# Performance work log

Measured on AMD Instinct MI355X. Metric: run time of the kernel, lower is better.

## Reference

```python
import jax, jax.numpy as jnp
import numpy as np

DN = ('NCDHW', 'OIDHW', 'NCDHW')  # torch Conv3d layout

def conv3d(x, w, b, pad):
    y = jax.lax.conv_general_dilated(x, w, (1, 1, 1), [(p, p) for p in pad], dimension_numbers=DN)
    return y + b[None, :, None, None, None]

def setup_inputs() -> dict:
    key = jax.random.key(0)
    ks = jax.random.split(key, 10)
    C, Cq = 64, 8  # in_channels, in_channels // 8
    s = 0.05
    x = jax.random.normal(ks[0], (2, C, 16, 16, 16), dtype=jnp.float32)
    return {
        'x': x,
        'wq': jax.random.normal(ks[1], (Cq, C, 1, 3, 1), jnp.float32) * s,
        'bq': jax.random.normal(ks[2], (Cq,), jnp.float32) * s,
        'wk': jax.random.normal(ks[3], (Cq, C, 3, 1, 1), jnp.float32) * s,
        'bk': jax.random.normal(ks[4], (Cq,), jnp.float32) * s,
        'wj': jax.random.normal(ks[5], (Cq, C, 1, 1, 3), jnp.float32) * s,
        'bj': jax.random.normal(ks[6], (Cq,), jnp.float32) * s,
        'wv': jax.random.normal(ks[7], (C, C, 1, 1, 1), jnp.float32) * s,
        'bv': jax.random.normal(ks[8], (C,), jnp.float32) * s,
        'gamma': jax.random.normal(ks[9], (1,), jnp.float32) * s,
    }

def reference(x, wq, bq, wk, bk, wj, bj, wv, bv, gamma):
    B, C, H, W, D = x.shape
    N = H * W * D
    q = conv3d(x, wq, bq, (0, 1, 0)).reshape(B, -1, N)   # [B, c, N]
    k = conv3d(x, wk, bk, (1, 0, 0)).reshape(B, -1, N)   # [B, c, N]
    j = conv3d(x, wj, bj, (0, 0, 1)).reshape(B, -1, N)   # [B, c, N]
    # affinity = (Q^T K) (J^T K) reassociated as Q^T (K J^T) K  -- identical math,
    # O(N^2 c) instead of O(N^3) since c = C//8 << N.
    kj = jnp.einsum('bcn,bdn->bcd', k, j)                # [B, c, c] = K @ J^T
    aff = jnp.einsum('bcn,bcd,bdm->bnm', q, kj, k)       # [B, N, N]
    aff = jax.nn.softmax(aff, axis=-1)
    v = conv3d(x, wv, bv, (0, 0, 0)).reshape(B, C, N)    # [B, C, N]
    weights = jnp.einsum('bcn,bnm->bcm', v, aff).reshape(B, C, H, W, D)
    return gamma * weights + x
```

## Files before the change

### kernel.cpp

```cpp
#include <hip/hip_runtime.h>

#define N 4096
#define CIN 64
#define NB 2

typedef unsigned short u16;
typedef short bf16x8 __attribute__((ext_vector_type(8)));
typedef float f32x4 __attribute__((ext_vector_type(4)));

#define OFF_QT 0
#define OFF_KT (OFF_QT + NB*N*8)
#define OFF_JT (OFF_KT + NB*N*8)
#define OFF_V  (OFF_JT + NB*N*8)
#define OFF_QK (OFF_V + NB*CIN*N)
#define OFF_MX (OFF_QK + NB*N*8)
#define OFF_SC (OFF_MX + NB*N)
#define OFF_KJ (OFF_SC + NB*N)

__device__ __forceinline__ u16 f2bf(float f) {
    union { float f; unsigned u; } v; v.f = f;
    unsigned r = (v.u + 0x7fffu + ((v.u >> 16) & 1u)) >> 16;
    return (u16)r;
}

__global__ __launch_bounds__(512, 4) void prep(
        const float* __restrict__ x,
        const float* __restrict__ wq, const float* __restrict__ bq,
        const float* __restrict__ wk, const float* __restrict__ bk,
        const float* __restrict__ wj, const float* __restrict__ bj,
        const float* __restrict__ wv, const float* __restrict__ bv,
        float* __restrict__ ws, u16* __restrict__ vbf, float* __restrict__ out) {
    __shared__ union {
        float kj2[2][8][256];
        float q1[8][256];
        float accv[256][8];
    } sh;
    __shared__ float kjpart[4][64];
    const int t    = threadIdx.x;
    const int tn   = t & 255;
    const int half = t >> 8;
    const int y    = blockIdx.y;
    const int bx   = blockIdx.x;
    const int b    = blockIdx.z;
    const int n    = bx * 256 + tn;
    const float* xb = x + (size_t)b * CIN * N + n;
    const int c0base = half * 32;

    if (y == 8) {
        const int lane = t & 63, wid = t >> 6;
        int d = n & 15, h = n >> 8;
        int ohl = (h > 0) ? -256 : 0, ohh = (h < 15) ? 256 : 0;
        int odl = (d > 0) ? -1 : 0,   odh = (d < 15) ? 1 : 0;
        float mhl = (h > 0) ? 1.f : 0.f, mhh = (h < 15) ? 1.f : 0.f;
        float mdl = (d > 0) ? 1.f : 0.f, mdh = (d < 15) ? 1.f : 0.f;
        float k[8], j[8];
#pragma unroll
        for (int cq = 0; cq < 8; ++cq) {
            k[cq] = half ? 0.f : bk[cq];
            j[cq] = half ? 0.f : bj[cq];
        }
        for (int c0i = 0; c0i < 32; c0i += 4) {
            const int c0 = c0base + c0i;
            float xc[4], xhl[4], xhh[4], xdl[4], xdh[4];
#pragma unroll
            for (int u = 0; u < 4; ++u) {
                const float* p = xb + (size_t)(c0 + u) * N;
                xc[u]  = p[0];
                xhl[u] = p[ohl]; xhh[u] = p[ohh];
                xdl[u] = p[odl]; xdh[u] = p[odh];
            }
#pragma unroll
            for (int u = 0; u < 4; ++u) {
                xhl[u] *= mhl; xhh[u] *= mhh;
                xdl[u] *= mdl; xdh[u] *= mdh;
            }
#pragma unroll
            for (int cq = 0; cq < 8; ++cq) {
                const float4* wk4 = (const float4*)(wk + (cq * CIN + c0) * 3);
                float4 ka4 = wk4[0], kb4 = wk4[1], kc4 = wk4[2];
                k[cq] += ka4.x * xhl[0] + ka4.y * xc[0] + ka4.z * xhh[0]
                       + ka4.w * xhl[1] + kb4.x * xc[1] + kb4.y * xhh[1]
                       + kb4.z * xhl[2] + kb4.w * xc[2] + kc4.x * xhh[2]
                       + kc4.y * xhl[3] + kc4.z * xc[3] + kc4.w * xhh[3];
                const float4* wj4 = (const float4*)(wj + (cq * CIN + c0) * 3);
                float4 ja4 = wj4[0], jb4 = wj4[1], jc4 = wj4[2];
                j[cq] += ja4.x * xdl[0] + ja4.y * xc[0] + ja4.z * xdh[0]
                       + ja4.w * xdl[1] + jb4.x * xc[1] + jb4.y * xdh[1]
                       + jb4.z * xdl[2] + jb4.w * xc[2] + jc4.x * xdh[2]
                       + jc4.y * xdl[3] + jc4.z * xc[3] + jc4.w * xdh[3];
            }
        }
        if (half) {
#pragma unroll
            for (int cq = 0; cq < 8; ++cq) {
                sh.kj2[0][cq][tn] = k[cq];
                sh.kj2[1][cq][tn] = j[cq];
            }
        }
        __syncthreads();
        if (!half) {
#pragma unroll
            for (int cq = 0; cq < 8; ++cq) {
                k[cq] += sh.kj2[0][cq][tn];
                j[cq] += sh.kj2[1][cq][tn];
            }
            size_t base = (size_t)(b * N + n) * 8;
#pragma unroll
            for (int cq = 0; cq < 8; ++cq) {
                ws[OFF_KT + base + cq] = k[cq];
                ws[OFF_JT + base + cq] = j[cq];
            }
#pragma unroll
            for (int g = 0; g < 4; ++g) {
                float a16[16];
#pragma unroll
                for (int cc = 0; cc < 2; ++cc)
#pragma unroll
                    for (int dd = 0; dd < 8; ++dd)
                        a16[cc * 8 + dd] = k[g * 2 + cc] * j[dd];
#pragma unroll
                for (int s = 32; s >= 1; s >>= 1)
#pragma unroll
                    for (int i = 0; i < 16; ++i) a16[i] += __shfl_down(a16[i], s, 64);
                if (lane == 0) {
#pragma unroll
                    for (int i = 0; i < 16; ++i) kjpart[wid][g * 16 + i] = a16[i];
                }
            }
        }
        __syncthreads();
        if (t < 64) {
            float s = kjpart[0][t] + kjpart[1][t] + kjpart[2][t] + kjpart[3][t];
            ws[OFF_KJ + (size_t)(b * 16 + bx) * 64 + t] = s;
        }
    } else if (y == 9) {
        int w = (n >> 4) & 15;
        int owl = (w > 0) ? -16 : 0, owh = (w < 15) ? 16 : 0;
        float mwl = (w > 0) ? 1.f : 0.f, mwh = (w < 15) ? 1.f : 0.f;
        float q[8];
#pragma unroll
        for (int cq = 0; cq < 8; ++cq) q[cq] = half ? 0.f : bq[cq];
        for (int c0i = 0; c0i < 32; c0i += 8) {
            const int c0 = c0base + c0i;
            float xc[8], xwl[8], xwh[8];
#pragma unroll
            for (int u = 0; u < 8; ++u) {
                const float* p = xb + (size_t)(c0 + u) * N;
                xc[u] = p[0]; xwl[u] = p[owl]; xwh[u] = p[owh];
            }
#pragma unroll
            for (int u = 0; u < 8; ++u) { xwl[u] *= mwl; xwh[u] *= mwh; }
#pragma unroll
            for (int cq = 0; cq < 8; ++cq) {
                const float4* w4 = (const float4*)(wq + (cq * CIN + c0) * 3);
                float4 a4 = w4[0], b4 = w4[1], c4 = w4[2],
                       d4 = w4[3], e4 = w4[4], f4 = w4[5];
                q[cq] += a4.x * xwl[0] + a4.y * xc[0] + a4.z * xwh[0]
                       + a4.w * xwl[1] + b4.x * xc[1] + b4.y * xwh[1]
                       + b4.z * xwl[2] + b4.w * xc[2] + c4.x * xwh[2]
                       + c4.y * xwl[3] + c4.z * xc[3] + c4.w * xwh[3]
                       + d4.x * xwl[4] + d4.y * xc[4] + d4.z * xwh[4]
                       + d4.w * xwl[5] + e4.x * xc[5] + e4.y * xwh[5]
                       + e4.z * xwl[6] + e4.w * xc[6] + f4.x * xwh[6]
                       + f4.y * xwl[7] + f4.z * xc[7] + f4.w * xwh[7];
            }
        }
        if (half) {
#pragma unroll
            for (int cq = 0; cq < 8; ++cq) sh.q1[cq][tn] = q[cq];
        }
        __syncthreads();
        if (!half) {
            size_t base = (size_t)(b * N + n) * 8;
#pragma unroll
            for (int cq = 0; cq < 8; ++cq)
                ws[OFF_QT + base + cq] = q[cq] + sh.q1[cq][tn];
        }
    } else {
        int yy = y;
        int co0 = yy * 8;
        float acc[8];
#pragma unroll
        for (int i = 0; i < 8; ++i) acc[i] = half ? 0.f : bv[co0 + i];
        for (int c0i = 0; c0i < 32; c0i += 8) {
            const int c0 = c0base + c0i;
            float xv[8];
#pragma unroll
            for (int u = 0; u < 8; ++u) xv[u] = xb[(size_t)(c0 + u) * N];
#pragma unroll
            for (int u = 0; u < 8; ++u)
#pragma unroll
                for (int i = 0; i < 8; ++i)
                    acc[i] += wv[(co0 + i) * CIN + c0 + u] * xv[u];
            if ((c0 >> 3) == yy) {
#pragma unroll
                for (int u = 0; u < 8; ++u)
                    out[(size_t)(b * CIN + c0 + u) * N + n] = xv[u];
            }
        }
        if (half) {
#pragma unroll
            for (int i = 0; i < 8; ++i) sh.accv[tn][i] = acc[i];
        }
        __syncthreads();
        if (!half) {
#pragma unroll
            for (int i = 0; i < 8; ++i)
                vbf[(size_t)(b * CIN + co0 + i) * N + n] = f2bf(acc[i] + sh.accv[tn][i]);
        }
    }
}

__global__ __launch_bounds__(512, 4) void pass1(const float* __restrict__ ws_in,
                                                float* __restrict__ ws,
                                                const float* __restrict__ gamma) {
    __shared__ float kjs[64];
    __shared__ float smx[8][4];
    __shared__ float ssum[8][4];
    const int t = threadIdx.x, lane = t & 63, wid = t >> 6;
    const int r0 = blockIdx.x * 4;
    const int b  = r0 >> 12;
    const float* ktb = ws_in + OFF_KT + (size_t)b * N * 8;

    if (t < 64) {
        const float* kjw = ws_in + OFF_KJ + (size_t)b * 16 * 64;
        float s = 0.f;
#pragma unroll
        for (int p = 0; p < 16; ++p) s += kjw[p * 64 + t];
        kjs[t] = s;
    }
    __syncthreads();

    float4 qa[4], qb[4];
#pragma unroll
    for (int rr = 0; rr < 4; ++rr) {
        const float4* q4 = (const float4*)(ws_in + OFF_QT + (size_t)(r0 + rr) * 8);
        float4 a4 = q4[0], b4 = q4[1];
        float qv[8] = {a4.x, a4.y, a4.z, a4.w, b4.x, b4.y, b4.z, b4.w};
        float o[8];
#pragma unroll
        for (int dd = 0; dd < 8; ++dd) {
            float a = 0.f;
#pragma unroll
            for (int c = 0; c < 8; ++c) a += qv[c] * kjs[c * 8 + dd];
            o[dd] = a;
        }
        qa[rr] = make_float4(o[0], o[1], o[2], o[3]);
        qb[rr] = make_float4(o[4], o[5], o[6], o[7]);
    }
    if (wid == 0 && lane < 32) {
        const int rr = lane >> 3, dd = lane & 7;
        const float* qr = ws_in + OFF_QT + (size_t)(r0 + rr) * 8;
        float o = 0.f;
#pragma unroll
        for (int c = 0; c < 8; ++c) o += qr[c] * kjs[c * 8 + dd];
        ws[OFF_QK + (size_t)r0 * 8 + lane] = o;
    }

    float as[4][8];
#pragma unroll
    for (int i = 0; i < 8; ++i) {
        const int m = wid * 512 + i * 64 + lane;
        const float4* kk4 = (const float4*)(ktb + (size_t)m * 8);
        float4 ka = kk4[0], kb2 = kk4[1];
#pragma unroll
        for (int rr = 0; rr < 4; ++rr)
            as[rr][i] = qa[rr].x * ka.x + qa[rr].y * ka.y + qa[rr].z * ka.z + qa[rr].w * ka.w
                      + qb[rr].x * kb2.x + qb[rr].y * kb2.y + qb[rr].z * kb2.z + qb[rr].w * kb2.w;
    }

    float mx[4];
#pragma unroll
    for (int rr = 0; rr < 4; ++rr) {
        float m01 = fmaxf(fmaxf(as[rr][0], as[rr][1]), fmaxf(as[rr][2], as[rr][3]));
        float m23 = fmaxf(fmaxf(as[rr][4], as[rr][5]), fmaxf(as[rr][6], as[rr][7]));
        mx[rr] = fmaxf(m01, m23);
    }
#pragma unroll
    for (int s = 32; s >= 1; s >>= 1)
#pragma unroll
        for (int rr = 0; rr < 4; ++rr)
            mx[rr] = fmaxf(mx[rr], __shfl_xor(mx[rr], s, 64));
    if (lane == 0) {
#pragma unroll
        for (int rr = 0; rr < 4; ++rr) smx[wid][rr] = mx[rr];
    }
    __syncthreads();
    float gm[4];
#pragma unroll
    for (int rr = 0; rr < 4; ++rr) {
        float g0 = fmaxf(fmaxf(smx[0][rr], smx[1][rr]), fmaxf(smx[2][rr], smx[3][rr]));
        float g1 = fmaxf(fmaxf(smx[4][rr], smx[5][rr]), fmaxf(smx[6][rr], smx[7][rr]));
        gm[rr] = fmaxf(g0, g1);
    }

    float sm[4];
#pragma unroll
    for (int rr = 0; rr < 4; ++rr) {
        float s0 = __expf(as[rr][0] - gm[rr]) + __expf(as[rr][1] - gm[rr])
                 + __expf(as[rr][2] - gm[rr]) + __expf(as[rr][3] - gm[rr]);
        float s1 = __expf(as[rr][4] - gm[rr]) + __expf(as[rr][5] - gm[rr])
                 + __expf(as[rr][6] - gm[rr]) + __expf(as[rr][7] - gm[rr]);
        sm[rr] = s0 + s1;
    }
#pragma unroll
    for (int s = 32; s >= 1; s >>= 1)
#pragma unroll
        for (int rr = 0; rr < 4; ++rr)
            sm[rr] += __shfl_xor(sm[rr], s, 64);
    if (lane == 0) {
#pragma unroll
        for (int rr = 0; rr < 4; ++rr) ssum[wid][rr] = sm[rr];
    }
    __syncthreads();
    if (t < 4) {
        float g0 = fmaxf(fmaxf(smx[0][t], smx[1][t]), fmaxf(smx[2][t], smx[3][t]));
        float g1 = fmaxf(fmaxf(smx[4][t], smx[5][t]), fmaxf(smx[6][t], smx[7][t]));
        float g  = fmaxf(g0, g1);
        float tt = ((ssum[0][t] + ssum[1][t]) + (ssum[2][t] + ssum[3][t]))
                 + ((ssum[4][t] + ssum[5][t]) + (ssum[6][t] + ssum[7][t]));
        ws[OFF_MX + r0 + t] = g;
        ws[OFF_SC + r0 + t] = gamma[0] / tt;
    }
}

__global__ __launch_bounds__(256) void pass2(const float* __restrict__ ws,
                                             const u16* __restrict__ vbf,
                                             float* __restrict__ out) {
    __shared__ u16 Pt[64][72];
    __shared__ u16 Vt[64][72];
    __shared__ float ks[64][8];
    const int t  = threadIdx.x;
    const int b  = blockIdx.z;
    const int m0 = blockIdx.x * 64;
    const int ns = blockIdx.y;
    const float* qkT = ws + OFF_QK + (size_t)b * N * 8;
    const float* ktb = ws + OFF_KT + (size_t)b * N * 8;
    const float* mxv = ws + OFF_MX + (size_t)b * N;
    const float* scv = ws + OFF_SC + (size_t)b * N;
    const u16*   vb  = vbf + (size_t)b * CIN * N;

    if (t < 128) ((float4*)ks)[t] = ((const float4*)(ktb + (size_t)m0 * 8))[t];

    const int lane = t & 63;
    const int wid  = t >> 6;
    const int l16  = lane & 15;
    const int lq   = lane >> 4;
    const int vc   = t >> 3;
    const int vseg = t & 7;

    f32x4 acc[4];
#pragma unroll
    for (int i = 0; i < 4; ++i) acc[i] = (f32x4){0.f, 0.f, 0.f, 0.f};

    for (int ch = 0; ch < 8; ++ch) {
        const int n0 = ns * 512 + ch * 64;
        const int n  = n0 + lane;
        const float4* q4 = (const float4*)(qkT + (size_t)n * 8);
        float4 qa = q4[0], qb = q4[1];
        float mxl = mxv[n], sl = scv[n];
        uint4 v0 = *(const uint4*)(vb + (size_t)vc        * N + n0 + vseg * 8);
        uint4 v1 = *(const uint4*)(vb + (size_t)(vc + 32) * N + n0 + vseg * 8);
        __syncthreads();
#pragma unroll
        for (int r = 0; r < 16; ++r) {
            int mi = wid * 16 + r;
            float4 k0 = *(const float4*)&ks[mi][0];
            float4 k1 = *(const float4*)&ks[mi][4];
            float a = qa.x * k0.x + qa.y * k0.y + qa.z * k0.z + qa.w * k0.w
                    + qb.x * k1.x + qb.y * k1.y + qb.z * k1.z + qb.w * k1.w;
            Pt[mi][lane] = f2bf(__expf(a - mxl) * sl);
        }
        *(uint4*)&Vt[vc][vseg * 8]      = v0;
        *(uint4*)&Vt[vc + 32][vseg * 8] = v1;
        __syncthreads();
#pragma unroll
        for (int kk = 0; kk < 2; ++kk) {
            int k0i = kk * 32 + lq * 8;
            bf16x8 bfrag = *(const bf16x8*)&Pt[wid * 16 + l16][k0i];
#pragma unroll
            for (int ct = 0; ct < 4; ++ct) {
                bf16x8 afrag = *(const bf16x8*)&Vt[ct * 16 + l16][k0i];
                acc[ct] = __builtin_amdgcn_mfma_f32_16x16x32_bf16(afrag, bfrag, acc[ct], 0, 0, 0);
            }
        }
    }
    float* ob = out + (size_t)b * CIN * N;
    const int mcol = m0 + wid * 16 + l16;
#pragma unroll
    for (int ct = 0; ct < 4; ++ct)
#pragma unroll
        for (int r = 0; r < 4; ++r) {
            int c = ct * 16 + lq * 4 + r;
            atomicAdd(&ob[(size_t)c * N + mcol], acc[ct][r]);
        }
}

extern "C" void kernel_launch(void* const* d_in, const int* in_sizes, int n_in,
                              void* d_out, int out_size, void* d_ws, size_t ws_size,
                              hipStream_t stream) {
    const float* x  = (const float*)d_in[0];
    const float* wq = (const float*)d_in[1];
    const float* bq = (const float*)d_in[2];
    const float* wk = (const float*)d_in[3];
    const float* bk = (const float*)d_in[4];
    const float* wj = (const float*)d_in[5];
    const float* bj = (const float*)d_in[6];
    const float* wv = (const float*)d_in[7];
    const float* bv = (const float*)d_in[8];
    const float* gamma = (const float*)d_in[9];
    float* ws  = (float*)d_ws;
    float* out = (float*)d_out;
    u16* vbf = (u16*)(ws + OFF_V);

    prep<<<dim3(16, 10, 2), 512, 0, stream>>>(x, wq, bq, wk, bk, wj, bj, wv, bv, ws, vbf, out);
    pass1<<<2048, 512, 0, stream>>>(ws, ws, gamma);
    pass2<<<dim3(64, 8, 2), 256, 0, stream>>>(ws, vbf, out);
}
```

Before: 160.2 us.

## Split Q/K/J conv blocks into 64-point tiles with 8-way channel split

```diff
diff --git a/kernel.cpp b/kernel.cpp
--- a/kernel.cpp
+++ b/kernel.cpp
@@ -31,78 +31,120 @@
         const float* __restrict__ wv, const float* __restrict__ bv,
         float* __restrict__ ws, u16* __restrict__ vbf, float* __restrict__ out) {
     __shared__ union {
-        float kj2[2][8][256];
-        float q1[8][256];
+        float ab[2][8][8][64];
         float accv[256][8];
     } sh;
-    __shared__ float kjpart[4][64];
-    const int t    = threadIdx.x;
-    const int tn   = t & 255;
-    const int half = t >> 8;
-    const int y    = blockIdx.y;
-    const int bx   = blockIdx.x;
-    const int b    = blockIdx.z;
-    const int n    = bx * 256 + tn;
-    const float* xb = x + (size_t)b * CIN * N + n;
-    const int c0base = half * 32;
-
-    if (y == 8) {
-        const int lane = t & 63, wid = t >> 6;
+    const int t   = threadIdx.x;
+    const int blk = blockIdx.x;
+    const int b   = blk >> 8;
+    const int r   = blk & 255;
+
+    if (r < 128) {
+        const int tn   = t & 255;
+        const int half = t >> 8;
+        const int yy   = r >> 4;
+        const int bx   = r & 15;
+        const int n    = bx * 256 + tn;
+        const float* xb = x + (size_t)b * CIN * N + n;
+        const int c0base = half * 32;
+        int co0 = yy * 8;
+        float acc[8];
+#pragma unroll
+        for (int i = 0; i < 8; ++i) acc[i] = half ? 0.f : bv[co0 + i];
+        for (int c0i = 0; c0i < 32; c0i += 8) {
+            const int c0 = c0base + c0i;
+            float xv[8];
+#pragma unroll
+            for (int u = 0; u < 8; ++u) xv[u] = xb[(size_t)(c0 + u) * N];
+#pragma unroll
+            for (int u = 0; u < 8; ++u)
+#pragma unroll
+                for (int i = 0; i < 8; ++i)
+                    acc[i] += wv[(co0 + i) * CIN + c0 + u] * xv[u];
+            if ((c0 >> 3) == yy) {
+#pragma unroll
+                for (int u = 0; u < 8; ++u)
+                    out[(size_t)(b * CIN + c0 + u) * N + n] = xv[u];
+            }
+        }
+        if (half) {
+#pragma unroll
+            for (int i = 0; i < 8; ++i) sh.accv[tn][i] = acc[i];
+        }
+        __syncthreads();
+        if (!half) {
+#pragma unroll
+            for (int i = 0; i < 8; ++i)
+                vbf[(size_t)(b * CIN + co0 + i) * N + n] = f2bf(acc[i] + sh.accv[tn][i]);
+        }
+    } else if (r < 192) {
+        const int bx  = r - 128;
+        const int tn  = t & 63;
+        const int oct = t >> 6;
+        const int n   = bx * 64 + tn;
+        const float* xb = x + (size_t)b * CIN * N + n;
+        const int c0 = oct * 8;
         int d = n & 15, h = n >> 8;
         int ohl = (h > 0) ? -256 : 0, ohh = (h < 15) ? 256 : 0;
         int odl = (d > 0) ? -1 : 0,   odh = (d < 15) ? 1 : 0;
         float mhl = (h > 0) ? 1.f : 0.f, mhh = (h < 15) ? 1.f : 0.f;
         float mdl = (d > 0) ? 1.f : 0.f, mdh = (d < 15) ? 1.f : 0.f;
+
+        float xc[8], xhl[8], xhh[8], xdl[8], xdh[8];
+#pragma unroll
+        for (int u = 0; u < 8; ++u) {
+            const float* p = xb + (size_t)(c0 + u) * N;
+            xc[u]  = p[0];
+            xhl[u] = p[ohl]; xhh[u] = p[ohh];
+            xdl[u] = p[odl]; xdh[u] = p[odh];
+        }
+#pragma unroll
+        for (int u = 0; u < 8; ++u) {
+            xhl[u] *= mhl; xhh[u] *= mhh;
+            xdl[u] *= mdl; xdh[u] *= mdh;
+        }
         float k[8], j[8];
 #pragma unroll
         for (int cq = 0; cq < 8; ++cq) {
-            k[cq] = half ? 0.f : bk[cq];
-            j[cq] = half ? 0.f : bj[cq];
-        }
-        for (int c0i = 0; c0i < 32; c0i += 4) {
-            const int c0 = c0base + c0i;
-            float xc[4], xhl[4], xhh[4], xdl[4], xdh[4];
-#pragma unroll
-            for (int u = 0; u < 4; ++u) {
-                const float* p = xb + (size_t)(c0 + u) * N;
-                xc[u]  = p[0];
-                xhl[u] = p[ohl]; xhh[u] = p[ohh];
-                xdl[u] = p[odl]; xdh[u] = p[odh];
-            }
-#pragma unroll
-            for (int u = 0; u < 4; ++u) {
-                xhl[u] *= mhl; xhh[u] *= mhh;
-                xdl[u] *= mdl; xdh[u] *= mdh;
-            }
+            const float4* wk4 = (const float4*)(wk + (cq * CIN + c0) * 3);
+            float4 a4 = wk4[0], b4 = wk4[1], c4 = wk4[2],
+                   d4 = wk4[3], e4 = wk4[4], f4 = wk4[5];
+            k[cq] = a4.x * xhl[0] + a4.y * xc[0] + a4.z * xhh[0]
+                  + a4.w * xhl[1] + b4.x * xc[1] + b4.y * xhh[1]
+                  + b4.z * xhl[2] + b4.w * xc[2] + c4.x * xhh[2]
+                  + c4.y * xhl[3] + c4.z * xc[3] + c4.w * xhh[3]
+                  + d4.x * xhl[4] + d4.y * xc[4] + d4.z * xhh[4]
+                  + d4.w * xhl[5] + e4.x * xc[5] + e4.y * xhh[5]
+                  + e4.z * xhl[6] + e4.w * xc[6] + f4.x * xhh[6]
+                  + f4.y * xhl[7] + f4.z * xc[7] + f4.w * xhh[7];
+            const float4* wj4 = (const float4*)(wj + (cq * CIN + c0) * 3);
+            float4 g4 = wj4[0], h4 = wj4[1], i4 = wj4[2],
+                   l4 = wj4[3], m4 = wj4[4], o4 = wj4[5];
+            j[cq] = g4.x * xdl[0] + g4.y * xc[0] + g4.z * xdh[0]
+                  + g4.w * xdl[1] + h4.x * xc[1] + h4.y * xdh[1]
+                  + h4.z * xdl[2] + h4.w * xc[2] + i4.x * xdh[2]
+                  + i4.y * xdl[3] + i4.z * xc[3] + i4.w * xdh[3]
+                  + l4.x * xdl[4] + l4.y * xc[4] + l4.z * xdh[4]
+                  + l4.w * xdl[5] + m4.x * xc[5] + m4.y * xdh[5]
+                  + m4.z * xdl[6] + m4.w * xc[6] + o4.x * xdh[6]
+                  + o4.y * xdl[7] + o4.z * xc[7] + o4.w * xdh[7];
+        }
+#pragma unroll
+        for (int cq = 0; cq < 8; ++cq) {
+            sh.ab[0][cq][oct][tn] = k[cq];
+            sh.ab[1][cq][oct][tn] = j[cq];
+        }
+        __syncthreads();
+        if (oct == 0) {
 #pragma unroll
             for (int cq = 0; cq < 8; ++cq) {
-                const float4* wk4 = (const float4*)(wk + (cq * CIN + c0) * 3);
-                float4 ka4 = wk4[0], kb4 = wk4[1], kc4 = wk4[2];
-                k[cq] += ka4.x * xhl[0] + ka4.y * xc[0] + ka4.z * xhh[0]
-                       + ka4.w * xhl[1] + kb4.x * xc[1] + kb4.y * xhh[1]
-                       + kb4.z * xhl[2] + kb4.w * xc[2] + kc4.x * xhh[2]
-                       + kc4.y * xhl[3] + kc4.z * xc[3] + kc4.w * xhh[3];
-                const float4* wj4 = (const float4*)(wj + (cq * CIN + c0) * 3);
-                float4 ja4 = wj4[0], jb4 = wj4[1], jc4 = wj4[2];
-                j[cq] += ja4.x * xdl[0] + ja4.y * xc[0] + ja4.z * xdh[0]
-                       + ja4.w * xdl[1] + jb4.x * xc[1] + jb4.y * xdh[1]
-                       + jb4.z * xdl[2] + jb4.w * xc[2] + jc4.x * xdh[2]
-                       + jc4.y * xdl[3] + jc4.z * xc[3] + jc4.w * xdh[3];
-            }
-        }
-        if (half) {
-#pragma unroll
-            for (int cq = 0; cq < 8; ++cq) {
-                sh.kj2[0][cq][tn] = k[cq];
-                sh.kj2[1][cq][tn] = j[cq];
-            }
-        }
-        __syncthreads();
-        if (!half) {
-#pragma unroll
-            for (int cq = 0; cq < 8; ++cq) {
-                k[cq] += sh.kj2[0][cq][tn];
-                j[cq] += sh.kj2[1][cq][tn];
+                float ks2 = bk[cq], js2 = bj[cq];
+#pragma unroll
+                for (int o = 0; o < 8; ++o) {
+                    ks2 += sh.ab[0][cq][o][tn];
+                    js2 += sh.ab[1][cq][o][tn];
+                }
+                k[cq] = ks2; j[cq] = js2;
             }
             size_t base = (size_t)(b * N + n) * 8;
 #pragma unroll
@@ -122,91 +164,59 @@
                 for (int s = 32; s >= 1; s >>= 1)
 #pragma unroll
                     for (int i = 0; i < 16; ++i) a16[i] += __shfl_down(a16[i], s, 64);
-                if (lane == 0) {
-#pragma unroll
-                    for (int i = 0; i < 16; ++i) kjpart[wid][g * 16 + i] = a16[i];
+                if (tn == 0) {
+#pragma unroll
+                    for (int i = 0; i < 16; ++i)
+                        ws[OFF_KJ + (size_t)(b * 64 + bx) * 64 + g * 16 + i] = a16[i];
                 }
             }
         }
-        __syncthreads();
-        if (t < 64) {
-            float s = kjpart[0][t] + kjpart[1][t] + kjpart[2][t] + kjpart[3][t];
-            ws[OFF_KJ + (size_t)(b * 16 + bx) * 64 + t] = s;
-        }
-    } else if (y == 9) {
+    } else {
+        const int bx  = r - 192;
+        const int tn  = t & 63;
+        const int oct = t >> 6;
+        const int n   = bx * 64 + tn;
+        const float* xb = x + (size_t)b * CIN * N + n;
+        const int c0 = oct * 8;
         int w = (n >> 4) & 15;
         int owl = (w > 0) ? -16 : 0, owh = (w < 15) ? 16 : 0;
         float mwl = (w > 0) ? 1.f : 0.f, mwh = (w < 15) ? 1.f : 0.f;
+
+        float xc[8], xwl[8], xwh[8];
+#pragma unroll
+        for (int u = 0; u < 8; ++u) {
+            const float* p = xb + (size_t)(c0 + u) * N;
+            xc[u] = p[0]; xwl[u] = p[owl]; xwh[u] = p[owh];
+        }
+#pragma unroll
+        for (int u = 0; u < 8; ++u) { xwl[u] *= mwl; xwh[u] *= mwh; }
         float q[8];
 #pragma unroll
-        for (int cq = 0; cq < 8; ++cq) q[cq] = half ? 0.f : bq[cq];
-        for (int c0i = 0; c0i < 32; c0i += 8) {
-            const int c0 = c0base + c0i;
-            float xc[8], xwl[8], xwh[8];
-#pragma unroll
-            for (int u = 0; u < 8; ++u) {
-                const float* p = xb + (size_t)(c0 + u) * N;
-                xc[u] = p[0]; xwl[u] = p[owl]; xwh[u] = p[owh];
-            }
-#pragma unroll
-            for (int u = 0; u < 8; ++u) { xwl[u] *= mwl; xwh[u] *= mwh; }
+        for (int cq = 0; cq < 8; ++cq) {
+            const float4* w4 = (const float4*)(wq + (cq * CIN + c0) * 3);
+            float4 a4 = w4[0], b4 = w4[1], c4 = w4[2],
+                   d4 = w4[3], e4 = w4[4], f4 = w4[5];
+            q[cq] = a4.x * xwl[0] + a4.y * xc[0] + a4.z * xwh[0]
+                  + a4.w * xwl[1] + b4.x * xc[1] + b4.y * xwh[1]
+                  + b4.z * xwl[2] + b4.w * xc[2] + c4.x * xwh[2]
+                  + c4.y * xwl[3] + c4.z * xc[3] + c4.w * xwh[3]
+                  + d4.x * xwl[4] + d4.y * xc[4] + d4.z * xwh[4]
+                  + d4.w * xwl[5] + e4.x * xc[5] + e4.y * xwh[5]
+                  + e4.z * xwl[6] + e4.w * xc[6] + f4.x * xwh[6]
+                  + f4.y * xwl[7] + f4.z * xc[7] + f4.w * xwh[7];
+        }
+#pragma unroll
+        for (int cq = 0; cq < 8; ++cq) sh.ab[0][cq][oct][tn] = q[cq];
+        __syncthreads();
+        if (oct == 0) {
+            size_t base = (size_t)(b * N + n) * 8;
 #pragma unroll
             for (int cq = 0; cq < 8; ++cq) {
-                const float4* w4 = (const float4*)(wq + (cq * CIN + c0) * 3);
-                float4 a4 = w4[0], b4 = w4[1], c4 = w4[2],
-                       d4 = w4[3], e4 = w4[4], f4 = w4[5];
-                q[cq] += a4.x * xwl[0] + a4.y * xc[0] + a4.z * xwh[0]
-                       + a4.w * xwl[1] + b4.x * xc[1] + b4.y * xwh[1]
-                       + b4.z * xwl[2] + b4.w * xc[2] + c4.x * xwh[2]
-                       + c4.y * xwl[3] + c4.z * xc[3] + c4.w * xwh[3]
-                       + d4.x * xwl[4] + d4.y * xc[4] + d4.z * xwh[4]
-                       + d4.w * xwl[5] + e4.x * xc[5] + e4.y * xwh[5]
-                       + e4.z * xwl[6] + e4.w * xc[6] + f4.x * xwh[6]
-                       + f4.y * xwl[7] + f4.z * xc[7] + f4.w * xwh[7];
-            }
-        }
-        if (half) {
-#pragma unroll
-            for (int cq = 0; cq < 8; ++cq) sh.q1[cq][tn] = q[cq];
-        }
-        __syncthreads();
-        if (!half) {
-            size_t base = (size_t)(b * N + n) * 8;
-#pragma unroll
-            for (int cq = 0; cq < 8; ++cq)
-                ws[OFF_QT + base + cq] = q[cq] + sh.q1[cq][tn];
-        }
-    } else {
-        int yy = y;
-        int co0 = yy * 8;
-        float acc[8];
-#pragma unroll
-        for (int i = 0; i < 8; ++i) acc[i] = half ? 0.f : bv[co0 + i];
-        for (int c0i = 0; c0i < 32; c0i += 8) {
-            const int c0 = c0base + c0i;
-            float xv[8];
-#pragma unroll
-            for (int u = 0; u < 8; ++u) xv[u] = xb[(size_t)(c0 + u) * N];
-#pragma unroll
-            for (int u = 0; u < 8; ++u)
-#pragma unroll
-                for (int i = 0; i < 8; ++i)
-                    acc[i] += wv[(co0 + i) * CIN + c0 + u] * xv[u];
-            if ((c0 >> 3) == yy) {
-#pragma unroll
-                for (int u = 0; u < 8; ++u)
-                    out[(size_t)(b * CIN + c0 + u) * N + n] = xv[u];
-            }
-        }
-        if (half) {
-#pragma unroll
-            for (int i = 0; i < 8; ++i) sh.accv[tn][i] = acc[i];
-        }
-        __syncthreads();
-        if (!half) {
-#pragma unroll
-            for (int i = 0; i < 8; ++i)
-                vbf[(size_t)(b * CIN + co0 + i) * N + n] = f2bf(acc[i] + sh.accv[tn][i]);
+                float qs = bq[cq];
+#pragma unroll
+                for (int o = 0; o < 8; ++o) qs += sh.ab[0][cq][o][tn];
+                ws[OFF_QT + base + cq] = qs;
+            }
         }
     }
 }
@@ -214,6 +224,7 @@
 __global__ __launch_bounds__(512, 4) void pass1(const float* __restrict__ ws_in,
                                                 float* __restrict__ ws,
                                                 const float* __restrict__ gamma) {
+    __shared__ float kj8[8][64];
     __shared__ float kjs[64];
     __shared__ float smx[8][4];
     __shared__ float ssum[8][4];
@@ -222,11 +233,19 @@
     const int b  = r0 >> 12;
     const float* ktb = ws_in + OFF_KT + (size_t)b * N * 8;
 
+    {
+        const int p8 = t >> 6, e = t & 63;
+        const float* kjw = ws_in + OFF_KJ + (size_t)b * 64 * 64;
+        float s = 0.f;
+#pragma unroll
+        for (int i = 0; i < 8; ++i) s += kjw[(p8 * 8 + i) * 64 + e];
+        kj8[p8][e] = s;
+    }
+    __syncthreads();
     if (t < 64) {
-        const float* kjw = ws_in + OFF_KJ + (size_t)b * 16 * 64;
         float s = 0.f;
 #pragma unroll
-        for (int p = 0; p < 16; ++p) s += kjw[p * 64 + t];
+        for (int p = 0; p < 8; ++p) s += kj8[p][t];
         kjs[t] = s;
     }
     __syncthreads();
@@ -413,7 +432,7 @@
     float* out = (float*)d_out;
     u16* vbf = (u16*)(ws + OFF_V);
 
-    prep<<<dim3(16, 10, 2), 512, 0, stream>>>(x, wq, bq, wk, bk, wj, bj, wv, bv, ws, vbf, out);
+    prep<<<dim3(512), 512, 0, stream>>>(x, wq, bq, wk, bk, wj, bj, wv, bv, ws, vbf, out);
     pass1<<<2048, 512, 0, stream>>>(ws, ws, gamma);
     pass2<<<dim3(64, 8, 2), 256, 0, stream>>>(ws, vbf, out);
 }
```

Result: faster. 145.4 us (-9.2%).
